# Kernel tuning notes

Measured on AMD Instinct MI355X. Metric: run time of the kernel, lower is better.

Reference implementation:

```python
import jax, jax.numpy as jnp
import numpy as np

DT_OVER_TAU = 20.0 / 100.0  # dt / tau from the module


def setup_inputs() -> dict:
    key = jax.random.key(0)
    k_u, k_m, k_n, k_wi, k_w = jax.random.split(key, 5)
    B, T, N, R = 1024, 1024, 256, 2
    u = jax.random.normal(k_u, (B, T), dtype=jnp.float32)
    m = jax.random.normal(k_m, (N, R), dtype=jnp.float32)          # std=1
    n = jax.random.normal(k_n, (N, R), dtype=jnp.float32)          # std=1
    wi = jax.random.normal(k_wi, (N,), dtype=jnp.float32)          # std=1
    w = 4.0 * jax.random.normal(k_w, (N, 1), dtype=jnp.float32)    # std=4
    return {"u": u, "m": m, "n": n, "wi": wi, "w": w}


def reference(u, m, n, wi, w):
    # u: [B, T]; m, n: [N, R]; wi: [N]; w: [N, 1]
    B, T = u.shape
    N = m.shape[0]
    inv_N = 1.0 / N
    w_vec = w[:, 0]  # [N]

    def step(x, u_t):
        # x: [B, N], u_t: [B]
        r = jnp.tanh(x)
        # low-rank recurrent drive: (r @ n) @ m.T / N  -> [B, N]
        rec = (r @ n) @ m.T * inv_N
        dx = (-x + rec + u_t[:, None] * wi[None, :]) * DT_OVER_TAU
        x_new = x + dx
        r_new = jnp.tanh(x_new)
        z_t = r_new @ w_vec * inv_N  # [B]
        return x_new, z_t

    x0 = jnp.zeros((B, N), dtype=u.dtype)
    _, z = jax.lax.scan(step, x0, u.T)  # z: [T, B]
    return z.T  # [B, T]
```

## Files before the change

### kernel.cpp

```cpp
#include <hip/hip_runtime.h>

#define T_LEN 1024

typedef float f2 __attribute__((ext_vector_type(2)));

__device__ __forceinline__ f2 sp(float x) { return (f2){x, x}; }

template<int CTRL>
__device__ __forceinline__ float dpp_add_f32(float v) {
    int mv = __builtin_amdgcn_update_dpp(0, __float_as_int(v), CTRL, 0xf, 0xf, true);
    return v + __int_as_float(mv);
}
__device__ __forceinline__ float rdl63(float p) {
    return __int_as_float(__builtin_amdgcn_readlane(__float_as_int(p), 63));
}

__global__ __launch_bounds__(256, 1) void rnn_lowrank_kernel(
    const float* __restrict__ u,
    const float* __restrict__ m,
    const float* __restrict__ n,
    const float* __restrict__ wi,
    const float* __restrict__ w,
    float* __restrict__ z)
{
    __shared__ float u_lds[4][T_LEN];

    const int wave = threadIdx.x >> 6;
    const int lane = threadIdx.x & 63;
    const int b    = (blockIdx.x << 2) + wave;

    const float dt   = 0.2f;
    const float invN = 1.0f / 256.0f;
    const float c    = 2.8853900817779268f;

    {
        const float4* src = reinterpret_cast<const float4*>(u + (size_t)b * T_LEN);
        float4*       dst = reinterpret_cast<float4*>(&u_lds[wave][0]);
#pragma unroll
        for (int k = 0; k < 4; ++k) {
            float4 v = src[lane + (k << 6)];
            v.x *= dt; v.y *= dt; v.z *= dt; v.w *= dt;
            dst[lane + (k << 6)] = v;
        }
    }

    const int j0 = lane, j1 = lane + 64, j2 = lane + 128, j3 = lane + 192;
    const float kn = dt * invN;
    const f2 m0_01 = (f2){m[2*j0+0]*c,  m[2*j1+0]*c };
    const f2 m0_23 = (f2){m[2*j2+0]*c,  m[2*j3+0]*c };
    const f2 m1_01 = (f2){m[2*j0+1]*c,  m[2*j1+1]*c };
    const f2 m1_23 = (f2){m[2*j2+1]*c,  m[2*j3+1]*c };
    const f2 wi_01 = (f2){wi[j0]*c,     wi[j1]*c    };
    const f2 wi_23 = (f2){wi[j2]*c,     wi[j3]*c    };
    const f2 n0_01 = (f2){n[2*j0+0]*kn, n[2*j1+0]*kn};
    const f2 n0_23 = (f2){n[2*j2+0]*kn, n[2*j3+0]*kn};
    const f2 n1_01 = (f2){n[2*j0+1]*kn, n[2*j1+1]*kn};
    const f2 n1_23 = (f2){n[2*j2+1]*kn, n[2*j3+1]*kn};
    const f2 w_01  = (f2){w[j0]*invN,   w[j1]*invN  };
    const f2 w_23  = (f2){w[j2]*invN,   w[j3]*invN  };

    float A = 0.0f, B = 0.0f, G = 0.0f;
    float a0 = 0.0f, a1 = 0.0f;
    float zbuf = 0.0f;
    float u_cur = u_lds[wave][0];

#pragma unroll 2
    for (int t = 0; t < T_LEN; ++t) {
        float u_next = u_lds[wave][(t + 1) & (T_LEN - 1)];
        G = fmaf(G, 0.8f, u_cur);
        f2 g01 = sp(G) * wi_01;
        f2 g23 = sp(G) * wi_23;

        A = fmaf(A, 0.8f, a0);
        B = fmaf(B, 0.8f, a1);

        f2 y01 = __builtin_elementwise_fma(sp(B), m1_01, g01);
        f2 y23 = __builtin_elementwise_fma(sp(B), m1_23, g23);
        y01 = __builtin_elementwise_fma(sp(A), m0_01, y01);
        y23 = __builtin_elementwise_fma(sp(A), m0_23, y23);

        f2 ex01, ex23;
        ex01.x = __builtin_amdgcn_exp2f(y01.x);
        ex01.y = __builtin_amdgcn_exp2f(y01.y);
        ex23.x = __builtin_amdgcn_exp2f(y23.x);
        ex23.y = __builtin_amdgcn_exp2f(y23.y);
        f2 d01 = ex01 + sp(1.0f);
        f2 d23 = ex23 + sp(1.0f);
        f2 rc01, rc23;
        rc01.x = __builtin_amdgcn_rcpf(d01.x);
        rc01.y = __builtin_amdgcn_rcpf(d01.y);
        rc23.x = __builtin_amdgcn_rcpf(d23.x);
        rc23.y = __builtin_amdgcn_rcpf(d23.y);
        f2 r01 = __builtin_elementwise_fma(sp(-2.0f), rc01, sp(1.0f));
        f2 r23 = __builtin_elementwise_fma(sp(-2.0f), rc23, sp(1.0f));

        f2 q0 = r01 * n0_01, q1 = r01 * n1_01, qz = r01 * w_01;
        q0 = __builtin_elementwise_fma(r23, n0_23, q0);
        q1 = __builtin_elementwise_fma(r23, n1_23, q1);
        qz = __builtin_elementwise_fma(r23, w_23,  qz);
        float p0 = q0.x + q0.y, p1 = q1.x + q1.y, pz = qz.x + qz.y;

#define RED3(CTRL)                      \
        p0 = dpp_add_f32<CTRL>(p0);     \
        p1 = dpp_add_f32<CTRL>(p1);     \
        pz = dpp_add_f32<CTRL>(pz);
        RED3(0x111)
        RED3(0x112)
        RED3(0x114)
        RED3(0x118)
        RED3(0x142)
        RED3(0x143)
#undef RED3

        a0 = rdl63(p0);
        a1 = rdl63(p1);
        float zs = rdl63(pz);

        zbuf = (lane == (t & 63)) ? zs : zbuf;
        if ((t & 63) == 63)
            z[(size_t)b * T_LEN + (t - 63) + lane] = zbuf;

        u_cur = u_next;
    }
}

extern "C" void kernel_launch(void* const* d_in, const int* in_sizes, int n_in,
                              void* d_out, int out_size, void* d_ws, size_t ws_size,
                              hipStream_t stream) {
    const float* u  = (const float*)d_in[0];
    const float* m  = (const float*)d_in[1];
    const float* n  = (const float*)d_in[2];
    const float* wi = (const float*)d_in[3];
    const float* w  = (const float*)d_in[4];
    float* z = (float*)d_out;

    dim3 grid(256), block(256);
    hipLaunchKernelGGL(rnn_lowrank_kernel, grid, block, 0, stream, u, m, n, wi, w, z);
}
```

Baseline: 204.7 us.

## Defer z reduction to batched LDS transpose-sum, use inline-asm DPP adds

Removes the z-output cross-lane DPP reduction from the serial per-step critical path. Each step now writes per-lane partial z sums into a 64x64 LDS tile, and every 64 steps each lane sums one row with a rotated index to avoid bank conflicts. The remaining two reductions use inline-asm v_add_f32_dpp so the DPP is fused into the add, and the unroll factor goes from 2 to 4. This adds 64KB of LDS, an LDS store every step and a periodic 64-element sum. Inline asm also hides dependencies from the compiler's hazard handling.

```diff
diff --git a/kernel.cpp b/kernel.cpp
--- a/kernel.cpp
+++ b/kernel.cpp
@@ -6,14 +6,13 @@
 
 __device__ __forceinline__ f2 sp(float x) { return (f2){x, x}; }
 
-template<int CTRL>
-__device__ __forceinline__ float dpp_add_f32(float v) {
-    int mv = __builtin_amdgcn_update_dpp(0, __float_as_int(v), CTRL, 0xf, 0xf, true);
-    return v + __int_as_float(mv);
-}
 __device__ __forceinline__ float rdl63(float p) {
     return __int_as_float(__builtin_amdgcn_readlane(__float_as_int(p), 63));
 }
+
+#define DPP_ADD(P, CTRL)                                                     \
+    asm("v_add_f32_dpp %0, %0, %0 " CTRL " row_mask:0xf bank_mask:0xf bound_ctrl:0" \
+        : "+v"(P))
 
 __global__ __launch_bounds__(256, 1) void rnn_lowrank_kernel(
     const float* __restrict__ u,
@@ -24,6 +23,7 @@
     float* __restrict__ z)
 {
     __shared__ float u_lds[4][T_LEN];
+    __shared__ float zmat[4][64][64];
 
     const int wave = threadIdx.x >> 6;
     const int lane = threadIdx.x & 63;
@@ -61,10 +61,9 @@
 
     float A = 0.0f, B = 0.0f, G = 0.0f;
     float a0 = 0.0f, a1 = 0.0f;
-    float zbuf = 0.0f;
     float u_cur = u_lds[wave][0];
 
-#pragma unroll 2
+#pragma unroll 4
     for (int t = 0; t < T_LEN; ++t) {
         float u_next = u_lds[wave][(t + 1) & (T_LEN - 1)];
         G = fmaf(G, 0.8f, u_cur);
@@ -98,27 +97,31 @@
         q0 = __builtin_elementwise_fma(r23, n0_23, q0);
         q1 = __builtin_elementwise_fma(r23, n1_23, q1);
         qz = __builtin_elementwise_fma(r23, w_23,  qz);
-        float p0 = q0.x + q0.y, p1 = q1.x + q1.y, pz = qz.x + qz.y;
+        float p0 = q0.x + q0.y, p1 = q1.x + q1.y;
 
-#define RED3(CTRL)                      \
-        p0 = dpp_add_f32<CTRL>(p0);     \
-        p1 = dpp_add_f32<CTRL>(p1);     \
-        pz = dpp_add_f32<CTRL>(pz);
-        RED3(0x111)
-        RED3(0x112)
-        RED3(0x114)
-        RED3(0x118)
-        RED3(0x142)
-        RED3(0x143)
-#undef RED3
+        zmat[wave][t & 63][lane] = qz.x + qz.y;
+
+        DPP_ADD(p0, "row_shr:1");  DPP_ADD(p1, "row_shr:1");
+        DPP_ADD(p0, "row_shr:2");  DPP_ADD(p1, "row_shr:2");
+        DPP_ADD(p0, "row_shr:4");  DPP_ADD(p1, "row_shr:4");
+        DPP_ADD(p0, "row_shr:8");  DPP_ADD(p1, "row_shr:8");
+        DPP_ADD(p0, "row_bcast:15"); DPP_ADD(p1, "row_bcast:15");
+        DPP_ADD(p0, "row_bcast:31"); DPP_ADD(p1, "row_bcast:31");
 
         a0 = rdl63(p0);
         a1 = rdl63(p1);
-        float zs = rdl63(pz);
 
-        zbuf = (lane == (t & 63)) ? zs : zbuf;
-        if ((t & 63) == 63)
-            z[(size_t)b * T_LEN + (t - 63) + lane] = zbuf;
+        if ((t & 63) == 63) {
+            float s0 = 0.0f, s1 = 0.0f, s2 = 0.0f, s3 = 0.0f;
+#pragma unroll
+            for (int k = 0; k < 64; k += 4) {
+                s0 += zmat[wave][lane][(lane + k + 0) & 63];
+                s1 += zmat[wave][lane][(lane + k + 1) & 63];
+                s2 += zmat[wave][lane][(lane + k + 2) & 63];
+                s3 += zmat[wave][lane][(lane + k + 3) & 63];
+            }
+            z[(size_t)b * T_LEN + (t - 63) + lane] = (s0 + s1) + (s2 + s3);
+        }
 
         u_cur = u_next;
     }
```

Measured after the change: 193.0 us. 1.06x faster.
